# Kernel optimization log

Measured on AMD Instinct MI355X. Metric: run time of the kernel, lower is better.

Reference implementation:

```python
import jax, jax.numpy as jnp
import numpy as np

N = 20000
E = 320000
IN_DIM = 128
HID = 64
HEADS = 8
OUT_DIM = 128
NEG_SLOPE = 0.2  # PyG GATConv default leaky_relu slope


def _glorot(key, shape):
    fan_in = shape[0] if len(shape) > 1 else shape[-1]
    return jax.random.normal(key, shape, dtype=jnp.float32) / jnp.sqrt(jnp.float32(fan_in))


def setup_inputs() -> dict:
    key = jax.random.key(0)
    ks = jax.random.split(key, 16)
    x = jax.random.normal(ks[0], (N, IN_DIM), dtype=jnp.float32)
    edge_index = jax.random.randint(ks[1], (2, E), 0, N, dtype=jnp.int32)
    HC = HEADS * HID
    return {
        "x": x,
        "edge_index": edge_index,
        # layer 1: in -> heads*hid (concat)
        "W1": _glorot(ks[2], (IN_DIM, HC)),
        "a_src1": _glorot(ks[3], (HEADS, HID)),
        "a_dst1": _glorot(ks[4], (HEADS, HID)),
        "b1": jnp.zeros((HC,), jnp.float32),
        # layer 2: heads*hid -> heads*hid (concat)
        "W2": _glorot(ks[5], (HC, HC)),
        "a_src2": _glorot(ks[6], (HEADS, HID)),
        "a_dst2": _glorot(ks[7], (HEADS, HID)),
        "b2": jnp.zeros((HC,), jnp.float32),
        # layer 3: heads*hid -> out, heads=1, concat=False
        "W3": _glorot(ks[8], (HC, OUT_DIM)),
        "a_src3": _glorot(ks[9], (1, OUT_DIM)),
        "a_dst3": _glorot(ks[10], (1, OUT_DIM)),
        "b3": jnp.zeros((OUT_DIM,), jnp.float32),
    }


def _gat_layer(x, src, dst, W, a_src, a_dst, b, heads, concat):
    # x: [N, F_in] -> h: [N, H, C]
    n = x.shape[0]
    h = (x @ W).reshape(n, heads, -1)
    # per-node attention half-logits: [N, H]
    al_src = jnp.sum(h * a_src[None], axis=-1)
    al_dst = jnp.sum(h * a_dst[None], axis=-1)
    # per-edge logits with leaky relu: [E, H]
    e = jax.nn.leaky_relu(al_src[src] + al_dst[dst], NEG_SLOPE)
    # segment softmax over incoming edges of each dst node
    emax = jax.ops.segment_max(e, dst, num_segments=n)
    ex = jnp.exp(e - emax[dst])
    den = jax.ops.segment_sum(ex, dst, num_segments=n)
    alpha = ex / (den[dst] + 1e-16)
    # weighted scatter-aggregate of source features: [E, H, C] -> [N, H, C]
    out = jax.ops.segment_sum(h[src] * alpha[:, :, None], dst, num_segments=n)
    out = out.reshape(n, -1) if concat else out.mean(axis=1)
    return out + b


def reference(x, edge_index, W1, a_src1, a_dst1, b1, W2, a_src2, a_dst2, b2,
              W3, a_src3, a_dst3, b3):
    # PyG GATConv adds self-loops by default
    loops = jnp.arange(N, dtype=edge_index.dtype)
    src = jnp.concatenate([edge_index[0], loops])
    dst = jnp.concatenate([edge_index[1], loops])
    # eval mode: dropout is identity
    h = _gat_layer(x, src, dst, W1, a_src1, a_dst1, b1, HEADS, True)
    h = jax.nn.elu(h)
    h = _gat_layer(h, src, dst, W2, a_src2, a_dst2, b2, HEADS, True)
    h = jax.nn.elu(h)
    out = _gat_layer(h, src, dst, W3, a_src3, a_dst3, b3, 1, False)
    return out
```

## Files before the change

kernel.cpp:

```cpp
#include <hip/hip_runtime.h>
#include <math.h>

#define NN 20000
#define EE 320000
#define ETOT 340000
#define NHEADS 8
#define HID 64
#define HCV 512
#define IND 128
#define OUTD 128
#define NEG_SLOPE 0.2f

typedef __attribute__((ext_vector_type(8))) short short8;
typedef __attribute__((ext_vector_type(8))) unsigned short ushort8;
typedef __attribute__((ext_vector_type(4))) float floatx4;

__device__ __forceinline__ ushort bf16_rne(float f) {
    union { float f; unsigned u; } v; v.f = f;
    unsigned u = v.u;
    unsigned r = (u + 0x7FFFu + ((u >> 16) & 1u)) >> 16;
    return (ushort)r;
}
__device__ __forceinline__ float bf16_to_f(ushort h) {
    union { unsigned u; float f; } v; v.u = ((unsigned)h) << 16;
    return v.f;
}

__device__ __forceinline__ void cvt_one(const float* W, ushort* Thi, ushort* Tlo,
                                        int idx, int K, int N) {
    int k = idx / N, n = idx - k * N;
    float f = W[idx];
    ushort hi = bf16_rne(f);
    ushort lo = bf16_rne(f - bf16_to_f(hi));
    Thi[(size_t)n * K + k] = hi;
    Tlo[(size_t)n * K + k] = lo;
}

#define S1 (IND * HCV)
#define S2 (HCV * HCV)
#define S3 (HCV * OUTD)
#define STOT (S1 + S2 + S3)
__global__ void prep_kernel(const float* __restrict__ W1, const float* __restrict__ W2,
                            const float* __restrict__ W3,
                            ushort* __restrict__ T1h, ushort* __restrict__ T1l,
                            ushort* __restrict__ T2h, ushort* __restrict__ T2l,
                            ushort* __restrict__ T3h, ushort* __restrict__ T3l,
                            int* __restrict__ cnt) {
    int idx = blockIdx.x * blockDim.x + threadIdx.x;
    if (idx < S1) cvt_one(W1, T1h, T1l, idx, IND, HCV);
    else if (idx < S1 + S2) cvt_one(W2, T2h, T2l, idx - S1, HCV, HCV);
    else if (idx < STOT) cvt_one(W3, T3h, T3l, idx - S1 - S2, HCV, OUTD);
    else if (idx < STOT + NN) cnt[idx - STOT] = 0;
}


__global__ void count_kernel(const int* __restrict__ ei, int* __restrict__ cnt) {
    int i = blockIdx.x * blockDim.x + threadIdx.x;
    if (i >= ETOT) return;
    int v = (i < EE) ? ei[EE + i] : (i - EE);
    atomicAdd(&cnt[v], 1);
}

#define SCH 20
__global__ __launch_bounds__(1024) void scan_kernel(const int* __restrict__ cnt,
                                                    int* __restrict__ row_ptr,
                                                    int* __restrict__ cursor) {
    __shared__ int wtot[16];
    __shared__ int woff[16];
    int t = threadIdx.x;
    int lane = t & 63;
    int wid = t >> 6;
    int base = t * SCH;
    int vals[SCH];
    int s = 0;
    #pragma unroll
    for (int i = 0; i < SCH; i++) {
        int idx = base + i;
        int v = (idx < NN) ? cnt[idx] : 0;
        vals[i] = v;
        s += v;
    }
    int incl = s;
    #pragma unroll
    for (int off = 1; off < 64; off <<= 1) {
        int u = __shfl_up(incl, off);
        if (lane >= off) incl += u;
    }
    int excl = incl - s;
    if (lane == 63) wtot[wid] = incl;
    __syncthreads();
    if (t == 0) {
        int run = 0;
        #pragma unroll
        for (int j = 0; j < 16; j++) { woff[j] = run; run += wtot[j]; }
        row_ptr[NN] = run;
    }
    __syncthreads();
    int run = woff[wid] + excl;
    #pragma unroll
    for (int i = 0; i < SCH; i++) {
        int idx = base + i;
        if (idx < NN) { row_ptr[idx] = run; cursor[idx] = run; run += vals[i]; }
    }
}

__global__ void fill_kernel(const int* __restrict__ ei, int* __restrict__ cursor,
                            int* __restrict__ csr_src) {
    int i = blockIdx.x * blockDim.x + threadIdx.x;
    if (i >= ETOT) return;
    int u, v;
    if (i < EE) { u = ei[i]; v = ei[EE + i]; }
    else        { u = i - EE; v = i - EE; }
    int pos = atomicAdd(&cursor[v], 1);
    csr_src[pos] = u;
}

#define LDK 40
template<bool SPLIT_A>
__global__ __launch_bounds__(256) void gemm128(const void* __restrict__ A_,
                                               const ushort* __restrict__ Bhi,
                                               const ushort* __restrict__ Blo,
                                               ushort* __restrict__ C16,
                                               const float* __restrict__ a_src,
                                               const float* __restrict__ a_dst,
                                               float* __restrict__ als,
                                               float* __restrict__ ald,
                                               int M, int K, int Nc) {
    __shared__ ushort sA[128 * LDK];
    __shared__ ushort sB[2][128 * LDK];
    int tid = threadIdx.x;
    int lane = tid & 63;
    int wv = tid >> 6;
    int wr = wv >> 1, wc = wv & 1;
    int m0 = blockIdx.x * 128, n0 = blockIdx.y * 128;
    int quad = lane >> 4;
    int l15 = lane & 15;
    int arow = tid >> 2;
    int ac4 = tid & 3;

    floatx4 acc[4][4] = {};
    const ushort* Ab = (const ushort*)A_;
    const float* Af = (const float*)A_;

    for (int k0 = 0; k0 < K; k0 += 32) {
        #pragma unroll
        for (int r = 0; r < 2; r++) {
            int row = arow + r * 64;
            int gm = m0 + row;
            if (SPLIT_A) {
                ushort8 h8;
                if (gm < M) {
                    float4 f0 = *(const float4*)&Af[(size_t)gm * K + k0 + ac4 * 8];
                    float4 f1 = *(const float4*)&Af[(size_t)gm * K + k0 + ac4 * 8 + 4];
                    float f[8] = {f0.x, f0.y, f0.z, f0.w, f1.x, f1.y, f1.z, f1.w};
                    #pragma unroll
                    for (int j = 0; j < 8; j++) h8[j] = bf16_rne(f[j]);
                } else {
                    #pragma unroll
                    for (int j = 0; j < 8; j++) h8[j] = 0;
                }
                *(ushort8*)&sA[row * LDK + ac4 * 8] = h8;
            } else {
                int4 va;
                if (gm < M) va = *(const int4*)&Ab[(size_t)gm * K + k0 + ac4 * 8];
                else        va = make_int4(0, 0, 0, 0);
                *(int4*)&sA[row * LDK + ac4 * 8] = va;
            }
            int gn = n0 + row;
            int4 bh = *(const int4*)&Bhi[(size_t)gn * K + k0 + ac4 * 8];
            int4 bl = *(const int4*)&Blo[(size_t)gn * K + k0 + ac4 * 8];
            *(int4*)&sB[0][row * LDK + ac4 * 8] = bh;
            *(int4*)&sB[1][row * LDK + ac4 * 8] = bl;
        }
        __syncthreads();
        short8 a[4], b_hi[4], b_lo[4];
        #pragma unroll
        for (int i = 0; i < 4; i++) {
            int am = wr * 64 + i * 16 + l15;
            a[i] = *(const short8*)&sA[am * LDK + quad * 8];
            int bn = wc * 64 + i * 16 + l15;
            b_hi[i] = *(const short8*)&sB[0][bn * LDK + quad * 8];
            b_lo[i] = *(const short8*)&sB[1][bn * LDK + quad * 8];
        }
        #pragma unroll
        for (int i = 0; i < 4; i++)
            #pragma unroll
            for (int j = 0; j < 4; j++) {
                acc[i][j] = __builtin_amdgcn_mfma_f32_16x16x32_bf16(a[i], b_hi[j], acc[i][j], 0, 0, 0);
                acc[i][j] = __builtin_amdgcn_mfma_f32_16x16x32_bf16(a[i], b_lo[j], acc[i][j], 0, 0, 0);
            }
        __syncthreads();
    }
    #pragma unroll
    for (int i = 0; i < 4; i++) {
        #pragma unroll
        for (int r = 0; r < 4; r++) {
            int gm = m0 + wr * 64 + i * 16 + quad * 4 + r;
            if (gm < M) {
                #pragma unroll
                for (int j = 0; j < 4; j++)
                    C16[(size_t)gm * Nc + n0 + wc * 64 + j * 16 + l15] = bf16_rne(acc[i][j][r]);
            }
        }
    }
    int hh = (n0 + wc * 64) >> 6;
    float as_v[4], ad_v[4];
    #pragma unroll
    for (int j = 0; j < 4; j++) {
        as_v[j] = a_src[hh * HID + j * 16 + l15];
        ad_v[j] = a_dst[hh * HID + j * 16 + l15];
    }
    #pragma unroll
    for (int i = 0; i < 4; i++) {
        #pragma unroll
        for (int r = 0; r < 4; r++) {
            float ps = 0.f, pd = 0.f;
            #pragma unroll
            for (int j = 0; j < 4; j++) {
                float cv = acc[i][j][r];
                ps = fmaf(cv, as_v[j], ps);
                pd = fmaf(cv, ad_v[j], pd);
            }
            #pragma unroll
            for (int off = 1; off <= 8; off <<= 1) {
                ps += __shfl_xor(ps, off);
                pd += __shfl_xor(pd, off);
            }
            if (l15 == 0) {
                int gm = m0 + wr * 64 + i * 16 + quad * 4 + r;
                if (gm < M) {
                    als[gm * NHEADS + hh] = ps;
                    ald[gm * NHEADS + hh] = pd;
                }
            }
        }
    }
}

__global__ __launch_bounds__(256) void gemm64x(const ushort* __restrict__ A,
                                               const ushort* __restrict__ Bhi,
                                               const ushort* __restrict__ Blo,
                                               float* __restrict__ C,
                                               const float* __restrict__ a_src,
                                               const float* __restrict__ a_dst,
                                               float* __restrict__ als,
                                               float* __restrict__ ald,
                                               int M, int K, int Nc) {
    __shared__ ushort sA[64 * LDK];
    __shared__ ushort sB[2][128 * LDK];
    __shared__ float psum_s[4][64];
    __shared__ float psum_d[4][64];
    int tid = threadIdx.x;
    int lane = tid & 63;
    int wv = tid >> 6;
    int m0 = blockIdx.x * 64;
    int quad = lane >> 4;
    int l15 = lane & 15;
    int arow = tid >> 2;
    int ac4 = tid & 3;

    floatx4 acc[4][2] = {};

    for (int k0 = 0; k0 < K; k0 += 32) {
        {
            int gm = m0 + arow;
            int4 va;
            if (gm < M) va = *(const int4*)&A[(size_t)gm * K + k0 + ac4 * 8];
            else        va = make_int4(0, 0, 0, 0);
            *(int4*)&sA[arow * LDK + ac4 * 8] = va;
            #pragma unroll
            for (int r = 0; r < 2; r++) {
                int gn = arow + r * 64;
                int4 bh = *(const int4*)&Bhi[(size_t)gn * K + k0 + ac4 * 8];
                int4 bl = *(const int4*)&Blo[(size_t)gn * K + k0 + ac4 * 8];
                *(int4*)&sB[0][(arow + r * 64) * LDK + ac4 * 8] = bh;
                *(int4*)&sB[1][(arow + r * 64) * LDK + ac4 * 8] = bl;
            }
        }
        __syncthreads();
        short8 a[4], b_hi[2], b_lo[2];
        #pragma unroll
        for (int i = 0; i < 4; i++) {
            int am = i * 16 + l15;
            a[i] = *(const short8*)&sA[am * LDK + quad * 8];
        }
        #pragma unroll
        for (int j = 0; j < 2; j++) {
            int bn = wv * 32 + j * 16 + l15;
            b_hi[j] = *(const short8*)&sB[0][bn * LDK + quad * 8];
            b_lo[j] = *(const short8*)&sB[1][bn * LDK + quad * 8];
        }
        #pragma unroll
        for (int i = 0; i < 4; i++)
            #pragma unroll
            for (int j = 0; j < 2; j++) {
                acc[i][j] = __builtin_amdgcn_mfma_f32_16x16x32_bf16(a[i], b_hi[j], acc[i][j], 0, 0, 0);
                acc[i][j] = __builtin_amdgcn_mfma_f32_16x16x32_bf16(a[i], b_lo[j], acc[i][j], 0, 0, 0);
            }
        __syncthreads();
    }
    #pragma unroll
    for (int i = 0; i < 4; i++) {
        #pragma unroll
        for (int r = 0; r < 4; r++) {
            int gm = m0 + i * 16 + quad * 4 + r;
            if (gm < M) {
                #pragma unroll
                for (int j = 0; j < 2; j++)
                    C[(size_t)gm * Nc + wv * 32 + j * 16 + l15] = acc[i][j][r];
            }
        }
    }
    float as_v[2], ad_v[2];
    #pragma unroll
    for (int j = 0; j < 2; j++) {
        as_v[j] = a_src[wv * 32 + j * 16 + l15];
        ad_v[j] = a_dst[wv * 32 + j * 16 + l15];
    }
    #pragma unroll
    for (int i = 0; i < 4; i++) {
        #pragma unroll
        for (int r = 0; r < 4; r++) {
            float ps = acc[i][0][r] * as_v[0] + acc[i][1][r] * as_v[1];
            float pd = acc[i][0][r] * ad_v[0] + acc[i][1][r] * ad_v[1];
            #pragma unroll
            for (int off = 1; off <= 8; off <<= 1) {
                ps += __shfl_xor(ps, off);
                pd += __shfl_xor(pd, off);
            }
            if (l15 == 0) {
                int row = i * 16 + quad * 4 + r;
                psum_s[wv][row] = ps;
                psum_d[wv][row] = pd;
            }
        }
    }
    __syncthreads();
    if (tid < 64) {
        int gm = m0 + tid;
        if (gm < M) {
            als[gm] = psum_s[0][tid] + psum_s[1][tid] + psum_s[2][tid] + psum_s[3][tid];
            ald[gm] = psum_d[0][tid] + psum_d[1][tid] + psum_d[2][tid] + psum_d[3][tid];
        }
    }
}

__global__ __launch_bounds__(256) void gather_kernel(const ushort* __restrict__ h,
                                                     const int* __restrict__ row_ptr,
                                                     const int* __restrict__ csr_src,
                                                     const float* __restrict__ als,
                                                     const float* __restrict__ ald,
                                                     const float* __restrict__ bias,
                                                     ushort* __restrict__ gout) {
    int lane = threadIdx.x & 63;
    int v = blockIdx.x * 4 + (threadIdx.x >> 6);
    if (v >= NN) return;
    int hd = lane >> 3;
    float adst = ald[v * NHEADS + hd];
    int s0 = row_ptr[v], s1 = row_ptr[v + 1];
    float acc[8] = {};
    float l = 0.f;
    int i = s0;
    for (; i + 4 <= s1; i += 4) {
        int u0 = csr_src[i], u1 = csr_src[i + 1], u2 = csr_src[i + 2], u3 = csr_src[i + 3];
        float t0 = als[u0 * NHEADS + hd] + adst;
        float t1 = als[u1 * NHEADS + hd] + adst;
        float t2 = als[u2 * NHEADS + hd] + adst;
        float t3 = als[u3 * NHEADS + hd] + adst;
        t0 = (t0 > 0.f) ? t0 : NEG_SLOPE * t0;
        t1 = (t1 > 0.f) ? t1 : NEG_SLOPE * t1;
        t2 = (t2 > 0.f) ? t2 : NEG_SLOPE * t2;
        t3 = (t3 > 0.f) ? t3 : NEG_SLOPE * t3;
        float p0 = __expf(fminf(t0, 80.f));
        float p1 = __expf(fminf(t1, 80.f));
        float p2 = __expf(fminf(t2, 80.f));
        float p3 = __expf(fminf(t3, 80.f));
        ushort8 x0 = *(const ushort8*)&h[(size_t)u0 * HCV + lane * 8];
        ushort8 x1 = *(const ushort8*)&h[(size_t)u1 * HCV + lane * 8];
        ushort8 x2 = *(const ushort8*)&h[(size_t)u2 * HCV + lane * 8];
        ushort8 x3 = *(const ushort8*)&h[(size_t)u3 * HCV + lane * 8];
        l += (p0 + p1) + (p2 + p3);
        #pragma unroll
        for (int j = 0; j < 8; j++) {
            acc[j] = fmaf(p0, bf16_to_f(x0[j]), acc[j]);
            acc[j] = fmaf(p1, bf16_to_f(x1[j]), acc[j]);
            acc[j] = fmaf(p2, bf16_to_f(x2[j]), acc[j]);
            acc[j] = fmaf(p3, bf16_to_f(x3[j]), acc[j]);
        }
    }
    for (; i < s1; i++) {
        int u0 = csr_src[i];
        float t0 = als[u0 * NHEADS + hd] + adst;
        t0 = (t0 > 0.f) ? t0 : NEG_SLOPE * t0;
        float p0 = __expf(fminf(t0, 80.f));
        ushort8 x0 = *(const ushort8*)&h[(size_t)u0 * HCV + lane * 8];
        l += p0;
        #pragma unroll
        for (int j = 0; j < 8; j++)
            acc[j] = fmaf(p0, bf16_to_f(x0[j]), acc[j]);
    }
    float inv = 1.f / (l + 1e-16f);
    ushort8 hv;
    #pragma unroll
    for (int j = 0; j < 8; j++) {
        float o = fmaf(acc[j], inv, bias[lane * 8 + j]);
        o = (o > 0.f) ? o : (__expf(o) - 1.f);
        hv[j] = bf16_rne(o);
    }
    *(ushort8*)&gout[(size_t)v * HCV + lane * 8] = hv;
}

__global__ __launch_bounds__(256) void gather3_kernel(const float* __restrict__ h,
                                                      const int* __restrict__ row_ptr,
                                                      const int* __restrict__ csr_src,
                                                      const float* __restrict__ als,
                                                      const float* __restrict__ ald,
                                                      const float* __restrict__ bias,
                                                      float* __restrict__ out) {
    int lane = threadIdx.x & 63;
    int v = blockIdx.x * 4 + (threadIdx.x >> 6);
    if (v >= NN) return;
    int e_sub = lane >> 5;
    int cg = lane & 31;
    float adst = ald[v];
    int s0 = row_ptr[v], s1 = row_ptr[v + 1];
    float m = -INFINITY;
    for (int i = s0 + e_sub; i < s1; i += 2) {
        int u = csr_src[i];
        float t = als[u] + adst;
        t = (t > 0.f) ? t : NEG_SLOPE * t;
        m = fmaxf(m, t);
    }
    m = fmaxf(m, __shfl_xor(m, 32));
    float4 acc = make_float4(0.f, 0.f, 0.f, 0.f);
    float l = 0.f;
    for (int i = s0 + e_sub; i < s1; i += 2) {
        int u = csr_src[i];
        float t = als[u] + adst;
        t = (t > 0.f) ? t : NEG_SLOPE * t;
        float p = __expf(t - m);
        float4 x = *(const float4*)&h[(size_t)u * OUTD + cg * 4];
        l += p;
        acc.x = fmaf(p, x.x, acc.x);
        acc.y = fmaf(p, x.y, acc.y);
        acc.z = fmaf(p, x.z, acc.z);
        acc.w = fmaf(p, x.w, acc.w);
    }
    l += __shfl_xor(l, 32);
    acc.x += __shfl_xor(acc.x, 32);
    acc.y += __shfl_xor(acc.y, 32);
    acc.z += __shfl_xor(acc.z, 32);
    acc.w += __shfl_xor(acc.w, 32);
    if (e_sub == 0) {
        float inv = 1.f / (l + 1e-16f);
        float4 b4 = *(const float4*)&bias[cg * 4];
        float4 o = make_float4(fmaf(acc.x, inv, b4.x), fmaf(acc.y, inv, b4.y),
                               fmaf(acc.z, inv, b4.z), fmaf(acc.w, inv, b4.w));
        *(float4*)&out[(size_t)v * OUTD + cg * 4] = o;
    }
}


extern "C" void kernel_launch(void* const* d_in, const int* in_sizes, int n_in,
                              void* d_out, int out_size, void* d_ws, size_t ws_size,
                              hipStream_t stream) {
    const float* x     = (const float*)d_in[0];
    const int*   ei    = (const int*)d_in[1];
    const float* W1    = (const float*)d_in[2];
    const float* as1   = (const float*)d_in[3];
    const float* ad1   = (const float*)d_in[4];
    const float* b1    = (const float*)d_in[5];
    const float* W2    = (const float*)d_in[6];
    const float* as2   = (const float*)d_in[7];
    const float* ad2   = (const float*)d_in[8];
    const float* b2    = (const float*)d_in[9];
    const float* W3    = (const float*)d_in[10];
    const float* as3   = (const float*)d_in[11];
    const float* ad3   = (const float*)d_in[12];
    const float* b3    = (const float*)d_in[13];
    float* out = (float*)d_out;

    size_t off = 0;
    auto carve = [&](size_t bytes) {
        void* p = (char*)d_ws + off;
        off += (bytes + 255) & ~(size_t)255;
        return p;
    };
    int* row_ptr  = (int*)carve((NN + 1) * sizeof(int));
    int* cursor   = (int*)carve(NN * sizeof(int));
    int* csr_src  = (int*)carve(ETOT * sizeof(int));
    ushort* hb16  = (ushort*)carve((size_t)NN * HCV * sizeof(ushort));
    float* bufA   = (float*)carve((size_t)NN * OUTD * sizeof(float));
    ushort* gact  = (ushort*)carve((size_t)NN * HCV * sizeof(ushort));
    float* als    = (float*)carve((size_t)NN * NHEADS * sizeof(float));
    float* ald    = (float*)carve((size_t)NN * NHEADS * sizeof(float));
    ushort* W1Th  = (ushort*)carve((size_t)S1 * sizeof(ushort));
    ushort* W1Tl  = (ushort*)carve((size_t)S1 * sizeof(ushort));
    ushort* W2Th  = (ushort*)carve((size_t)S2 * sizeof(ushort));
    ushort* W2Tl  = (ushort*)carve((size_t)S2 * sizeof(ushort));
    ushort* W3Th  = (ushort*)carve((size_t)S3 * sizeof(ushort));
    ushort* W3Tl  = (ushort*)carve((size_t)S3 * sizeof(ushort));
    (void)ws_size; (void)n_in; (void)in_sizes; (void)out_size;

    dim3 blk(256);

    prep_kernel<<<(STOT + NN + 255) / 256, blk, 0, stream>>>(W1, W2, W3,
        W1Th, W1Tl, W2Th, W2Tl, W3Th, W3Tl, cursor);

    count_kernel<<<(ETOT + 255) / 256, blk, 0, stream>>>(ei, cursor);
    scan_kernel<<<1, 1024, 0, stream>>>(cursor, row_ptr, cursor);
    fill_kernel<<<(ETOT + 255) / 256, blk, 0, stream>>>(ei, cursor, csr_src);

    int mt = (NN + 127) / 128;
    int mt64 = (NN + 63) / 64;
    int nwaves_n = (NN + 3) / 4;

    gemm128<true><<<dim3(mt, HCV / 128), blk, 0, stream>>>(x, W1Th, W1Tl,
        hb16, as1, ad1, als, ald, NN, IND, HCV);
    gather_kernel<<<nwaves_n, blk, 0, stream>>>(hb16, row_ptr, csr_src, als, ald, b1, gact);

    gemm128<false><<<dim3(mt, HCV / 128), blk, 0, stream>>>(gact, W2Th, W2Tl,
        hb16, as2, ad2, als, ald, NN, HCV, HCV);
    gather_kernel<<<nwaves_n, blk, 0, stream>>>(hb16, row_ptr, csr_src, als, ald, b2, gact);

    gemm64x<<<dim3(mt64, 1), blk, 0, stream>>>(gact, W3Th, W3Tl, bufA,
        as3, ad3, als, ald, NN, HCV, OUTD);
    gather3_kernel<<<nwaves_n, blk, 0, stream>>>(bufA, row_ptr, csr_src, als, ald, b3, out);
}
```

Baseline: 360.3 us.

## Switch GEMMs and activations from split-bf16 to single fp16 MFMA with 64-row tiles

Weights are now converted to a single fp16 copy instead of a bf16 hi/lo pair. This halves the MFMA count and the B-operand loads in all three GEMMs. Intermediate activations and features are stored as fp16 instead of bf16. The layer-1/2 GEMM tile shrinks from 128x128 to 64x128, with the per-head attention dot products reduced through shared memory, which doubles the number of blocks. The trade-off is lower mantissa accuracy in the weights and the narrower fp16 range, which could hurt accuracy or overflow on large activations.

```diff
diff --git a/kernel.cpp b/kernel.cpp
--- a/kernel.cpp
+++ b/kernel.cpp
@@ -11,29 +11,12 @@
 #define OUTD 128
 #define NEG_SLOPE 0.2f
 
-typedef __attribute__((ext_vector_type(8))) short short8;
-typedef __attribute__((ext_vector_type(8))) unsigned short ushort8;
+typedef __attribute__((ext_vector_type(8))) _Float16 half8;
 typedef __attribute__((ext_vector_type(4))) float floatx4;
 
-__device__ __forceinline__ ushort bf16_rne(float f) {
-    union { float f; unsigned u; } v; v.f = f;
-    unsigned u = v.u;
-    unsigned r = (u + 0x7FFFu + ((u >> 16) & 1u)) >> 16;
-    return (ushort)r;
-}
-__device__ __forceinline__ float bf16_to_f(ushort h) {
-    union { unsigned u; float f; } v; v.u = ((unsigned)h) << 16;
-    return v.f;
-}
-
-__device__ __forceinline__ void cvt_one(const float* W, ushort* Thi, ushort* Tlo,
-                                        int idx, int K, int N) {
+__device__ __forceinline__ void cvt_one(const float* W, _Float16* T, int idx, int K, int N) {
     int k = idx / N, n = idx - k * N;
-    float f = W[idx];
-    ushort hi = bf16_rne(f);
-    ushort lo = bf16_rne(f - bf16_to_f(hi));
-    Thi[(size_t)n * K + k] = hi;
-    Tlo[(size_t)n * K + k] = lo;
+    T[(size_t)n * K + k] = (_Float16)W[idx];
 }
 
 #define S1 (IND * HCV)
@@ -42,14 +25,12 @@
 #define STOT (S1 + S2 + S3)
 __global__ void prep_kernel(const float* __restrict__ W1, const float* __restrict__ W2,
                             const float* __restrict__ W3,
-                            ushort* __restrict__ T1h, ushort* __restrict__ T1l,
-                            ushort* __restrict__ T2h, ushort* __restrict__ T2l,
-                            ushort* __restrict__ T3h, ushort* __restrict__ T3l,
-                            int* __restrict__ cnt) {
+                            _Float16* __restrict__ T1, _Float16* __restrict__ T2,
+                            _Float16* __restrict__ T3, int* __restrict__ cnt) {
     int idx = blockIdx.x * blockDim.x + threadIdx.x;
-    if (idx < S1) cvt_one(W1, T1h, T1l, idx, IND, HCV);
-    else if (idx < S1 + S2) cvt_one(W2, T2h, T2l, idx - S1, HCV, HCV);
-    else if (idx < STOT) cvt_one(W3, T3h, T3l, idx - S1 - S2, HCV, OUTD);
+    if (idx < S1) cvt_one(W1, T1, idx, IND, HCV);
+    else if (idx < S1 + S2) cvt_one(W2, T2, idx - S1, HCV, HCV);
+    else if (idx < STOT) cvt_one(W3, T3, idx - S1 - S2, HCV, OUTD);
     else if (idx < STOT + NN) cnt[idx - STOT] = 0;
 }
 
@@ -117,137 +98,136 @@
 
 #define LDK 40
 template<bool SPLIT_A>
-__global__ __launch_bounds__(256) void gemm128(const void* __restrict__ A_,
-                                               const ushort* __restrict__ Bhi,
-                                               const ushort* __restrict__ Blo,
-                                               ushort* __restrict__ C16,
-                                               const float* __restrict__ a_src,
-                                               const float* __restrict__ a_dst,
-                                               float* __restrict__ als,
-                                               float* __restrict__ ald,
-                                               int M, int K, int Nc) {
-    __shared__ ushort sA[128 * LDK];
-    __shared__ ushort sB[2][128 * LDK];
+__global__ __launch_bounds__(256) void gemm_l12(const void* __restrict__ A_,
+                                                const _Float16* __restrict__ Bt,
+                                                _Float16* __restrict__ C16,
+                                                const float* __restrict__ a_src,
+                                                const float* __restrict__ a_dst,
+                                                float* __restrict__ als,
+                                                float* __restrict__ ald,
+                                                int M, int K) {
+    __shared__ _Float16 sA[64 * LDK];
+    __shared__ _Float16 sB[128 * LDK];
+    __shared__ float psum_s[4][64];
+    __shared__ float psum_d[4][64];
     int tid = threadIdx.x;
     int lane = tid & 63;
     int wv = tid >> 6;
-    int wr = wv >> 1, wc = wv & 1;
-    int m0 = blockIdx.x * 128, n0 = blockIdx.y * 128;
+    int m0 = blockIdx.x * 64, n0 = blockIdx.y * 128;
     int quad = lane >> 4;
     int l15 = lane & 15;
     int arow = tid >> 2;
     int ac4 = tid & 3;
 
-    floatx4 acc[4][4] = {};
-    const ushort* Ab = (const ushort*)A_;
+    floatx4 acc[4][2] = {};
+    const _Float16* Ah = (const _Float16*)A_;
     const float* Af = (const float*)A_;
 
     for (int k0 = 0; k0 < K; k0 += 32) {
-        #pragma unroll
-        for (int r = 0; r < 2; r++) {
-            int row = arow + r * 64;
-            int gm = m0 + row;
+        {
+            int gm = m0 + arow;
             if (SPLIT_A) {
-                ushort8 h8;
+                half8 h8;
                 if (gm < M) {
                     float4 f0 = *(const float4*)&Af[(size_t)gm * K + k0 + ac4 * 8];
                     float4 f1 = *(const float4*)&Af[(size_t)gm * K + k0 + ac4 * 8 + 4];
                     float f[8] = {f0.x, f0.y, f0.z, f0.w, f1.x, f1.y, f1.z, f1.w};
                     #pragma unroll
-                    for (int j = 0; j < 8; j++) h8[j] = bf16_rne(f[j]);
+                    for (int j = 0; j < 8; j++) h8[j] = (_Float16)f[j];
                 } else {
                     #pragma unroll
-                    for (int j = 0; j < 8; j++) h8[j] = 0;
+                    for (int j = 0; j < 8; j++) h8[j] = (_Float16)0.f;
                 }
-                *(ushort8*)&sA[row * LDK + ac4 * 8] = h8;
+                *(half8*)&sA[arow * LDK + ac4 * 8] = h8;
             } else {
                 int4 va;
-                if (gm < M) va = *(const int4*)&Ab[(size_t)gm * K + k0 + ac4 * 8];
+                if (gm < M) va = *(const int4*)&Ah[(size_t)gm * K + k0 + ac4 * 8];
                 else        va = make_int4(0, 0, 0, 0);
-                *(int4*)&sA[row * LDK + ac4 * 8] = va;
-            }
-            int gn = n0 + row;
-            int4 bh = *(const int4*)&Bhi[(size_t)gn * K + k0 + ac4 * 8];
-            int4 bl = *(const int4*)&Blo[(size_t)gn * K + k0 + ac4 * 8];
-            *(int4*)&sB[0][row * LDK + ac4 * 8] = bh;
-            *(int4*)&sB[1][row * LDK + ac4 * 8] = bl;
+                *(int4*)&sA[arow * LDK + ac4 * 8] = va;
+            }
+            #pragma unroll
+            for (int r = 0; r < 2; r++) {
+                int gn = n0 + arow + r * 64;
+                int4 vb = *(const int4*)&Bt[(size_t)gn * K + k0 + ac4 * 8];
+                *(int4*)&sB[(arow + r * 64) * LDK + ac4 * 8] = vb;
+            }
         }
         __syncthreads();
-        short8 a[4], b_hi[4], b_lo[4];
-        #pragma unroll
-        for (int i = 0; i < 4; i++) {
-            int am = wr * 64 + i * 16 + l15;
-            a[i] = *(const short8*)&sA[am * LDK + quad * 8];
-            int bn = wc * 64 + i * 16 + l15;
-            b_hi[i] = *(const short8*)&sB[0][bn * LDK + quad * 8];
-            b_lo[i] = *(const short8*)&sB[1][bn * LDK + quad * 8];
-        }
+        half8 a[4], b[2];
         #pragma unroll
         for (int i = 0; i < 4; i++)
-            #pragma unroll
-            for (int j = 0; j < 4; j++) {
-                acc[i][j] = __builtin_amdgcn_mfma_f32_16x16x32_bf16(a[i], b_hi[j], acc[i][j], 0, 0, 0);
-                acc[i][j] = __builtin_amdgcn_mfma_f32_16x16x32_bf16(a[i], b_lo[j], acc[i][j], 0, 0, 0);
-            }
+            a[i] = *(const half8*)&sA[(i * 16 + l15) * LDK + quad * 8];
+        #pragma unroll
+        for (int j = 0; j < 2; j++)
+            b[j] = *(const half8*)&sB[(wv * 32 + j * 16 + l15) * LDK + quad * 8];
+        #pragma unroll
+        for (int i = 0; i < 4; i++)
+            #pragma unroll
+            for (int j = 0; j < 2; j++)
+                acc[i][j] = __builtin_amdgcn_mfma_f32_16x16x32_f16(a[i], b[j], acc[i][j], 0, 0, 0);
         __syncthreads();
     }
     #pragma unroll
     for (int i = 0; i < 4; i++) {
         #pragma unroll
         for (int r = 0; r < 4; r++) {
-            int gm = m0 + wr * 64 + i * 16 + quad * 4 + r;
+            int gm = m0 + i * 16 + quad * 4 + r;
             if (gm < M) {
                 #pragma unroll
-                for (int j = 0; j < 4; j++)
-                    C16[(size_t)gm * Nc + n0 + wc * 64 + j * 16 + l15] = bf16_rne(acc[i][j][r]);
-            }
-        }
-    }
-    int hh = (n0 + wc * 64) >> 6;
-    float as_v[4], ad_v[4];
-    #pragma unroll
-    for (int j = 0; j < 4; j++) {
-        as_v[j] = a_src[hh * HID + j * 16 + l15];
-        ad_v[j] = a_dst[hh * HID + j * 16 + l15];
+                for (int j = 0; j < 2; j++)
+                    C16[(size_t)gm * HCV + n0 + wv * 32 + j * 16 + l15] = (_Float16)acc[i][j][r];
+            }
+        }
+    }
+    int h0 = n0 >> 6;
+    float as_v[2], ad_v[2];
+    #pragma unroll
+    for (int j = 0; j < 2; j++) {
+        int dim = (wv * 32 + j * 16 + l15) & 63;
+        int hh = h0 + (wv >> 1);
+        as_v[j] = a_src[hh * HID + dim];
+        ad_v[j] = a_dst[hh * HID + dim];
     }
     #pragma unroll
     for (int i = 0; i < 4; i++) {
         #pragma unroll
         for (int r = 0; r < 4; r++) {
-            float ps = 0.f, pd = 0.f;
-            #pragma unroll
-            for (int j = 0; j < 4; j++) {
-                float cv = acc[i][j][r];
-                ps = fmaf(cv, as_v[j], ps);
-                pd = fmaf(cv, ad_v[j], pd);
-            }
+            float ps = acc[i][0][r] * as_v[0] + acc[i][1][r] * as_v[1];
+            float pd = acc[i][0][r] * ad_v[0] + acc[i][1][r] * ad_v[1];
             #pragma unroll
             for (int off = 1; off <= 8; off <<= 1) {
                 ps += __shfl_xor(ps, off);
                 pd += __shfl_xor(pd, off);
             }
             if (l15 == 0) {
-                int gm = m0 + wr * 64 + i * 16 + quad * 4 + r;
-                if (gm < M) {
-                    als[gm * NHEADS + hh] = ps;
-                    ald[gm * NHEADS + hh] = pd;
-                }
-            }
-        }
-    }
-}
-
-__global__ __launch_bounds__(256) void gemm64x(const ushort* __restrict__ A,
-                                               const ushort* __restrict__ Bhi,
-                                               const ushort* __restrict__ Blo,
-                                               float* __restrict__ C,
-                                               const float* __restrict__ a_src,
-                                               const float* __restrict__ a_dst,
-                                               float* __restrict__ als,
-                                               float* __restrict__ ald,
-                                               int M, int K, int Nc) {
-    __shared__ ushort sA[64 * LDK];
-    __shared__ ushort sB[2][128 * LDK];
+                int row = i * 16 + quad * 4 + r;
+                psum_s[wv][row] = ps;
+                psum_d[wv][row] = pd;
+            }
+        }
+    }
+    __syncthreads();
+    if (tid < 64) {
+        int gm = m0 + tid;
+        if (gm < M) {
+            als[gm * NHEADS + h0]     = psum_s[0][tid] + psum_s[1][tid];
+            als[gm * NHEADS + h0 + 1] = psum_s[2][tid] + psum_s[3][tid];
+            ald[gm * NHEADS + h0]     = psum_d[0][tid] + psum_d[1][tid];
+            ald[gm * NHEADS + h0 + 1] = psum_d[2][tid] + psum_d[3][tid];
+        }
+    }
+}
+
+__global__ __launch_bounds__(256) void gemm3(const _Float16* __restrict__ A,
+                                             const _Float16* __restrict__ Bt,
+                                             float* __restrict__ C,
+                                             const float* __restrict__ a_src,
+                                             const float* __restrict__ a_dst,
+                                             float* __restrict__ als,
+                                             float* __restrict__ ald,
+                                             int M, int K) {
+    __shared__ _Float16 sA[64 * LDK];
+    __shared__ _Float16 sB[128 * LDK];
     __shared__ float psum_s[4][64];
     __shared__ float psum_d[4][64];
     int tid = threadIdx.x;
@@ -271,32 +251,23 @@
             #pragma unroll
             for (int r = 0; r < 2; r++) {
                 int gn = arow + r * 64;
-                int4 bh = *(const int4*)&Bhi[(size_t)gn * K + k0 + ac4 * 8];
-                int4 bl = *(const int4*)&Blo[(size_t)gn * K + k0 + ac4 * 8];
-                *(int4*)&sB[0][(arow + r * 64) * LDK + ac4 * 8] = bh;
-                *(int4*)&sB[1][(arow + r * 64) * LDK + ac4 * 8] = bl;
+                int4 vb = *(const int4*)&Bt[(size_t)gn * K + k0 + ac4 * 8];
+                *(int4*)&sB[(arow + r * 64) * LDK + ac4 * 8] = vb;
             }
         }
         __syncthreads();
-        short8 a[4], b_hi[2], b_lo[2];
-        #pragma unroll
-        for (int i = 0; i < 4; i++) {
-            int am = i * 16 + l15;
-            a[i] = *(const short8*)&sA[am * LDK + quad * 8];
-        }
-        #pragma unroll
-        for (int j = 0; j < 2; j++) {
-            int bn = wv * 32 + j * 16 + l15;
-            b_hi[j] = *(const short8*)&sB[0][bn * LDK + quad * 8];
-            b_lo[j] = *(const short8*)&sB[1][bn * LDK + quad * 8];
-        }
+        half8 a[4], b[2];
         #pragma unroll
         for (int i = 0; i < 4; i++)
-            #pragma unroll
-            for (int j = 0; j < 2; j++) {
-                acc[i][j] = __builtin_amdgcn_mfma_f32_16x16x32_bf16(a[i], b_hi[j], acc[i][j], 0, 0, 0);
-                acc[i][j] = __builtin_amdgcn_mfma_f32_16x16x32_bf16(a[i], b_lo[j], acc[i][j], 0, 0, 0);
-            }
+            a[i] = *(const half8*)&sA[(i * 16 + l15) * LDK + quad * 8];
+        #pragma unroll
+        for (int j = 0; j < 2; j++)
+            b[j] = *(const half8*)&sB[(wv * 32 + j * 16 + l15) * LDK + quad * 8];
+        #pragma unroll
+        for (int i = 0; i < 4; i++)
+            #pragma unroll
+            for (int j = 0; j < 2; j++)
+                acc[i][j] = __builtin_amdgcn_mfma_f32_16x16x32_f16(a[i], b[j], acc[i][j], 0, 0, 0);
         __syncthreads();
     }
     #pragma unroll
@@ -307,7 +278,7 @@
             if (gm < M) {
                 #pragma unroll
                 for (int j = 0; j < 2; j++)
-                    C[(size_t)gm * Nc + wv * 32 + j * 16 + l15] = acc[i][j][r];
+                    C[(size_t)gm * OUTD + wv * 32 + j * 16 + l15] = acc[i][j][r];
             }
         }
     }
@@ -345,13 +316,13 @@
     }
 }
 
-__global__ __launch_bounds__(256) void gather_kernel(const ushort* __restrict__ h,
+__global__ __launch_bounds__(256) void gather_kernel(const _Float16* __restrict__ h,
                                                      const int* __restrict__ row_ptr,
                                                      const int* __restrict__ csr_src,
                                                      const float* __restrict__ als,
                                                      const float* __restrict__ ald,
                                                      const float* __restrict__ bias,
-                                                     ushort* __restrict__ gout) {
+                                                     _Float16* __restrict__ gout) {
     int lane = threadIdx.x & 63;
     int v = blockIdx.x * 4 + (threadIdx.x >> 6);
     if (v >= NN) return;
@@ -375,17 +346,17 @@
         float p1 = __expf(fminf(t1, 80.f));
         float p2 = __expf(fminf(t2, 80.f));
         float p3 = __expf(fminf(t3, 80.f));
-        ushort8 x0 = *(const ushort8*)&h[(size_t)u0 * HCV + lane * 8];
-        ushort8 x1 = *(const ushort8*)&h[(size_t)u1 * HCV + lane * 8];
-        ushort8 x2 = *(const ushort8*)&h[(size_t)u2 * HCV + lane * 8];
-        ushort8 x3 = *(const ushort8*)&h[(size_t)u3 * HCV + lane * 8];
+        half8 x0 = *(const half8*)&h[(size_t)u0 * HCV + lane * 8];
+        half8 x1 = *(const half8*)&h[(size_t)u1 * HCV + lane * 8];
+        half8 x2 = *(const half8*)&h[(size_t)u2 * HCV + lane * 8];
+        half8 x3 = *(const half8*)&h[(size_t)u3 * HCV + lane * 8];
         l += (p0 + p1) + (p2 + p3);
         #pragma unroll
         for (int j = 0; j < 8; j++) {
-            acc[j] = fmaf(p0, bf16_to_f(x0[j]), acc[j]);
-            acc[j] = fmaf(p1, bf16_to_f(x1[j]), acc[j]);
-            acc[j] = fmaf(p2, bf16_to_f(x2[j]), acc[j]);
-            acc[j] = fmaf(p3, bf16_to_f(x3[j]), acc[j]);
+            acc[j] = fmaf(p0, (float)x0[j], acc[j]);
+            acc[j] = fmaf(p1, (float)x1[j], acc[j]);
+            acc[j] = fmaf(p2, (float)x2[j], acc[j]);
+            acc[j] = fmaf(p3, (float)x3[j], acc[j]);
         }
     }
     for (; i < s1; i++) {
@@ -393,21 +364,21 @@
         float t0 = als[u0 * NHEADS + hd] + adst;
         t0 = (t0 > 0.f) ? t0 : NEG_SLOPE * t0;
         float p0 = __expf(fminf(t0, 80.f));
-        ushort8 x0 = *(const ushort8*)&h[(size_t)u0 * HCV + lane * 8];
+        half8 x0 = *(const half8*)&h[(size_t)u0 * HCV + lane * 8];
         l += p0;
         #pragma unroll
         for (int j = 0; j < 8; j++)
-            acc[j] = fmaf(p0, bf16_to_f(x0[j]), acc[j]);
+            acc[j] = fmaf(p0, (float)x0[j], acc[j]);
     }
     float inv = 1.f / (l + 1e-16f);
-    ushort8 hv;
+    half8 hv;
     #pragma unroll
     for (int j = 0; j < 8; j++) {
         float o = fmaf(acc[j], inv, bias[lane * 8 + j]);
         o = (o > 0.f) ? o : (__expf(o) - 1.f);
-        hv[j] = bf16_rne(o);
-    }
-    *(ushort8*)&gout[(size_t)v * HCV + lane * 8] = hv;
+        hv[j] = (_Float16)o;
+    }
+    *(half8*)&gout[(size_t)v * HCV + lane * 8] = hv;
 }
 
 __global__ __launch_bounds__(256) void gather3_kernel(const float* __restrict__ h,
@@ -486,44 +457,40 @@
         off += (bytes + 255) & ~(size_t)255;
         return p;
     };
-    int* row_ptr  = (int*)carve((NN + 1) * sizeof(int));
-    int* cursor   = (int*)carve(NN * sizeof(int));
-    int* csr_src  = (int*)carve(ETOT * sizeof(int));
-    ushort* hb16  = (ushort*)carve((size_t)NN * HCV * sizeof(ushort));
-    float* bufA   = (float*)carve((size_t)NN * OUTD * sizeof(float));
-    ushort* gact  = (ushort*)carve((size_t)NN * HCV * sizeof(ushort));
-    float* als    = (float*)carve((size_t)NN * NHEADS * sizeof(float));
-    float* ald    = (float*)carve((size_t)NN * NHEADS * sizeof(float));
-    ushort* W1Th  = (ushort*)carve((size_t)S1 * sizeof(ushort));
-    ushort* W1Tl  = (ushort*)carve((size_t)S1 * sizeof(ushort));
-    ushort* W2Th  = (ushort*)carve((size_t)S2 * sizeof(ushort));
-    ushort* W2Tl  = (ushort*)carve((size_t)S2 * sizeof(ushort));
-    ushort* W3Th  = (ushort*)carve((size_t)S3 * sizeof(ushort));
-    ushort* W3Tl  = (ushort*)carve((size_t)S3 * sizeof(ushort));
+    int* row_ptr   = (int*)carve((NN + 1) * sizeof(int));
+    int* cursor    = (int*)carve(NN * sizeof(int));
+    int* csr_src   = (int*)carve(ETOT * sizeof(int));
+    _Float16* hf16 = (_Float16*)carve((size_t)NN * HCV * sizeof(_Float16));
+    float* bufA    = (float*)carve((size_t)NN * OUTD * sizeof(float));
+    _Float16* gact = (_Float16*)carve((size_t)NN * HCV * sizeof(_Float16));
+    float* als     = (float*)carve((size_t)NN * NHEADS * sizeof(float));
+    float* ald     = (float*)carve((size_t)NN * NHEADS * sizeof(float));
+    _Float16* W1T  = (_Float16*)carve((size_t)S1 * sizeof(_Float16));
+    _Float16* W2T  = (_Float16*)carve((size_t)S2 * sizeof(_Float16));
+    _Float16* W3T  = (_Float16*)carve((size_t)S3 * sizeof(_Float16));
     (void)ws_size; (void)n_in; (void)in_sizes; (void)out_size;
 
     dim3 blk(256);
 
     prep_kernel<<<(STOT + NN + 255) / 256, blk, 0, stream>>>(W1, W2, W3,
-        W1Th, W1Tl, W2Th, W2Tl, W3Th, W3Tl, cursor);
+        W1T, W2T, W3T, cursor);
 
     count_kernel<<<(ETOT + 255) / 256, blk, 0, stream>>>(ei, cursor);
     scan_kernel<<<1, 1024, 0, stream>>>(cursor, row_ptr, cursor);
     fill_kernel<<<(ETOT + 255) / 256, blk, 0, stream>>>(ei, cursor, csr_src);
 
-    int mt = (NN + 127) / 128;
     int mt64 = (NN + 63) / 64;
     int nwaves_n = (NN + 3) / 4;
 
-    gemm128<true><<<dim3(mt, HCV / 128), blk, 0, stream>>>(x, W1Th, W1Tl,
-        hb16, as1, ad1, als, ald, NN, IND, HCV);
-    gather_kernel<<<nwaves_n, blk, 0, stream>>>(hb16, row_ptr, csr_src, als, ald, b1, gact);
-
-    gemm128<false><<<dim3(mt, HCV / 128), blk, 0, stream>>>(gact, W2Th, W2Tl,
-        hb16, as2, ad2, als, ald, NN, HCV, HCV);
-    gather_kernel<<<nwaves_n, blk, 0, stream>>>(hb16, row_ptr, csr_src, als, ald, b2, gact);
-
-    gemm64x<<<dim3(mt64, 1), blk, 0, stream>>>(gact, W3Th, W3Tl, bufA,
-        as3, ad3, als, ald, NN, HCV, OUTD);
+    gemm_l12<true><<<dim3(mt64, HCV / 128), blk, 0, stream>>>(x, W1T,
+        hf16, as1, ad1, als, ald, NN, IND);
+    gather_kernel<<<nwaves_n, blk, 0, stream>>>(hf16, row_ptr, csr_src, als, ald, b1, gact);
+
+    gemm_l12<false><<<dim3(mt64, HCV / 128), blk, 0, stream>>>(gact, W2T,
+        hf16, as2, ad2, als, ald, NN, HCV);
+    gather_kernel<<<nwaves_n, blk, 0, stream>>>(hf16, row_ptr, csr_src, als, ald, b2, gact);
+
+    gemm3<<<dim3(mt64, 1), blk, 0, stream>>>(gact, W3T, bufA,
+        as3, ad3, als, ald, NN, HCV);
     gather3_kernel<<<nwaves_n, blk, 0, stream>>>(bufA, row_ptr, csr_src, als, ald, b3, out);
 }
```

New measurement: 346.3 us. 1.04x faster.
